# Kernel optimization log

Hardware: AMD Instinct MI355X
Metric: run time of the kernel (lower is better)

## Reference

```python
import jax, jax.numpy as jnp
import numpy as np

B = 2048

def _conv(x, w, b, stride):
    y = jax.lax.conv_general_dilated(x, w, (stride, stride), 'VALID',
                                     dimension_numbers=('NCHW', 'OIHW', 'NCHW'))
    return y + b[None, :, None, None]

def _local_conv(x, w, b):
    # w: (Ho, Wo, Co, Ci, kh, kw), b: (Ho, Wo, Co); stride 1, valid
    Ho, Wo, Co, Ci, kh, kw = w.shape
    # patches: (B, Ci, kh*kw, Ho, Wo) -- sliding windows, small fixed loop over kernel taps
    patches = jnp.stack([x[:, :, i:i + Ho, j:j + Wo]
                         for i in range(kh) for j in range(kw)], axis=2)
    wf = w.reshape(Ho, Wo, Co, Ci, kh * kw)
    y = jnp.einsum('bcphw,hwocp->bohw', patches, wf)
    return y + jnp.transpose(b, (2, 0, 1))[None]

def setup_inputs() -> dict:
    key = jax.random.key(0)
    ks = jax.random.split(key, 18)
    s = 0.05
    inp = {
        'x': jax.random.normal(ks[0], (B, 5, 60, 60), dtype=jnp.float32),
        'info': jax.random.normal(ks[1], (B, 8), dtype=jnp.float32),
        'w1': jax.random.normal(ks[2], (32, 5, 3, 3), dtype=jnp.float32) * s,
        'b1': jnp.zeros((32,), dtype=jnp.float32),
        'w2a': jax.random.normal(ks[3], (64, 32, 3, 3), dtype=jnp.float32) * s,
        'b2a': jnp.zeros((64,), dtype=jnp.float32),
        'w2b': jax.random.normal(ks[4], (64, 64, 3, 3), dtype=jnp.float32) * s,
        'b2b': jnp.zeros((64,), dtype=jnp.float32),
        'lw3': jax.random.normal(ks[5], (9, 9, 64, 64, 5, 5), dtype=jnp.float32) * s,
        'lb3': jnp.zeros((9, 9, 64), dtype=jnp.float32),
        'lw4': jax.random.normal(ks[6], (5, 5, 64, 64, 5, 5), dtype=jnp.float32) * s,
        'lb4': jnp.zeros((5, 5, 64), dtype=jnp.float32),
        'lw5': jax.random.normal(ks[7], (3, 3, 64, 64, 3, 3), dtype=jnp.float32) * s,
        'lb5': jnp.zeros((3, 3, 64), dtype=jnp.float32),
        'hw': jax.random.normal(ks[8], (2, 584), dtype=jnp.float32) * s,
        'hb': jnp.zeros((2,), dtype=jnp.float32),
    }
    return inp

def reference(x, info, w1, b1, w2a, b2a, w2b, b2b, lw3, lb3, lw4, lb4, lw5, lb5, hw, hb):
    h = jnp.tanh(_conv(x, w1, b1, 2))            # (B,32,29,29)
    h = jnp.tanh(_conv(h, w2a, b2a, 1))          # (B,64,27,27)
    h = jnp.tanh(_conv(h, w2b, b2b, 2))          # (B,64,13,13)
    h = jnp.tanh(_local_conv(h, lw3, lb3))       # (B,64,9,9)
    h = jnp.tanh(_local_conv(h, lw4, lb4))       # (B,64,5,5)
    h = jnp.tanh(_local_conv(h, lw5, lb5))       # (B,64,3,3)
    h = h.reshape(h.shape[0], -1)                # (B,576)
    h = jnp.concatenate([h, info], axis=1)       # (B,584)
    logits = h @ hw.T + hb                       # (B,2)
    return jax.nn.softmax(logits, axis=1)
```

## Files before the change

kernel.cpp:

```cpp
#include <hip/hip_runtime.h>
#include <stdint.h>

#define THREADS 256

typedef short bf16x8 __attribute__((ext_vector_type(8)));
typedef float f32x4 __attribute__((ext_vector_type(4)));
typedef unsigned uint2_ __attribute__((ext_vector_type(2)));

#define GPTR(x) ((const __attribute__((address_space(1))) void*)(x))
#define LPTR(x) ((__attribute__((address_space(3))) void*)(x))

__device__ __forceinline__ unsigned short f2bf(float v) {
  unsigned u = __builtin_bit_cast(unsigned, v);
  u = (u + 0x7fff + ((u >> 16) & 1)) >> 16;
  return (unsigned short)u;
}
__device__ __forceinline__ float bf2f(unsigned short h) {
  return __builtin_bit_cast(float, (unsigned)h << 16);
}
__device__ __forceinline__ float fast_tanh(float x) {
  return 1.f - 2.f / (__expf(2.f * x) + 1.f);
}

__device__ __forceinline__ int xcd_swizzle(int wg, int nwg) {
  const int q = nwg >> 3, rr = nwg & 7;
  const int xcd = wg & 7, l = wg >> 3;
  return (xcd < rr ? xcd * (q + 1) : rr * (q + 1) + (xcd - rr) * q) + l;
}

__global__ void pack_w1t(const float* __restrict__ w1, float* __restrict__ w1t) {
  int idx = blockIdx.x * THREADS + threadIdx.x;
  if (idx >= 45 * 32) return;
  int t = idx >> 5, co = idx & 31;
  w1t[t * 32 + co] = w1[co * 45 + t];
}

__global__ void __launch_bounds__(256) conv1_direct(
    const float* __restrict__ x, const float* __restrict__ w1t,
    const float* __restrict__ bias, unsigned short* __restrict__ out, int Bc,
    int bstart) {
  constexpr int CI = 5, CO = 32, IH = 60, IW = 60, OH = 29, OW = 29;
  constexpr int RPB = 2, NRB = 15;

  __shared__ float xs[CI * 5 * 60];

  const int tid = threadIdx.x;
  const int b = blockIdx.x / NRB;
  const int qb = blockIdx.x % NRB;
  const int oh0 = qb * RPB;
  const int rows = min(RPB, OH - oh0);
  const int ih0 = oh0 * 2;
  const int ihn = rows * 2 + 1;

  const float* xp = x + (size_t)(bstart + b) * (CI * IH * IW);

  const int nf4 = CI * ihn * 15;
  for (int i = tid; i < nf4; i += 256) {
    int col = i % 15;
    int row = i / 15;
    int ci = row / ihn, r = row % ihn;
    ((float4*)xs)[row * 15 + col] = ((const float4*)xp)[(ci * IH + ih0 + r) * 15 + col];
  }
  __syncthreads();

  const int lane = tid & 63;
  const int wu = __builtin_amdgcn_readfirstlane(tid >> 6);
  if (lane >= rows * OW) return;
  const int r = lane / OW, c = lane % OW;
  const int base = (r * 2) * 60 + c * 2;
  const int cstr = ihn * 60;

  float acc[8];
#pragma unroll
  for (int j = 0; j < 8; j++) acc[j] = bias[wu * 8 + j];

#pragma unroll
  for (int ci = 0; ci < CI; ci++)
#pragma unroll
    for (int kh = 0; kh < 3; kh++)
#pragma unroll
      for (int kw = 0; kw < 3; kw++) {
        const float v = xs[ci * cstr + base + kh * 60 + kw];
        const float* wt = w1t + ((ci * 3 + kh) * 3 + kw) * 32 + wu * 8;
#pragma unroll
        for (int j = 0; j < 8; j++) acc[j] = fmaf(v, wt[j], acc[j]);
      }

  const int p = (oh0 + r) * OW + c;
  bf16x8 o;
#pragma unroll
  for (int j = 0; j < 8; j++) o[j] = (short)f2bf(fast_tanh(acc[j]));
  *(bf16x8*)(out + ((size_t)p * Bc + b) * CO + wu * 8) = o;
}

template <int CI, int KS>
__global__ void __launch_bounds__(THREADS) pack_w(const float* __restrict__ w,
                                                  unsigned short* __restrict__ wp,
                                                  int npos) {
  constexpr int K = CI * KS * KS;
  constexpr int S = K / 32;
  int idx = blockIdx.x * THREADS + threadIdx.x;
  int total = npos * S * 2048;
  if (idx >= total) return;
  int e = idx & 7;
  int lane = (idx >> 3) & 63;
  int mt = (idx >> 9) & 3;
  int rest = idx >> 11;
  int s = rest % S, pos = rest / S;
  int co = mt * 16 + (lane & 15);
  int k = s * 32 + (lane >> 4) * 8 + e;
  int tap = k / CI, ci = k % CI;
  int kh = tap / KS, kw = tap % KS;
  float v = w[((((size_t)pos * 64 + co) * CI + ci) * KS + kh) * KS + kw];
  wp[idx] = f2bf(v);
}

template <int CI, int IH, int IW, int OH, int OW, int KS, int ST, bool LOCAL, int BT>
__global__ void __launch_bounds__(256) conv_mfma(
    const unsigned short* __restrict__ X, const unsigned short* __restrict__ Wp,
    const float* __restrict__ bias, unsigned short* __restrict__ Y, int Bc) {
  constexpr int S = CI * KS * KS / 32;
  constexpr int NPOS = OH * OW;
  constexpr int NJ = BT / 64;
  constexpr int NB = BT / 64;
  constexpr int NVM = 1 + NB;

  __shared__ unsigned short As[3][2048];
  __shared__ unsigned short Bs[3][BT * 32];

  const int tid = threadIdx.x;
  const int lane = tid & 63;
  const int wu = tid >> 6;
  const int n = lane & 15, g = lane >> 4;

  const int nbt = Bc / BT;
  int wg = xcd_swizzle(blockIdx.x, gridDim.x);
  int pos, btile;
  if (LOCAL) {
    btile = wg % nbt;
    pos = wg / nbt;
  } else {
    pos = wg % NPOS;
    btile = wg / NPOS;
  }
  const int oh = pos / OW, ow = pos % OW;
  const int b0 = btile * BT;

  const unsigned short* Wpp = Wp + (LOCAL ? (size_t)pos * (S * 2048) : 0);

  const int srow = tid >> 2;
  const int scol = (tid & 3) * 8;

  auto stage = [&](int s, int buf3) {
    __builtin_amdgcn_global_load_lds(GPTR(Wpp + s * 2048 + tid * 8),
                                     LPTR(&As[buf3][tid * 8]), 16, 0, 0);
    const int tap = (s * 32) / CI;
    const int ci0 = (s * 32) % CI;
    const int kh = tap / KS, kw = tap % KS;
    const int pin = (oh * ST + kh) * IW + (ow * ST + kw);
    const size_t base = (size_t)pin * Bc + b0;
#pragma unroll
    for (int i = 0; i < NB; i++)
      __builtin_amdgcn_global_load_lds(
          GPTR(X + (base + i * 64 + srow) * CI + ci0 + scol),
          LPTR(&Bs[buf3][i * 2048 + tid * 8]), 16, 0, 0);
  };

  f32x4 acc[4][NJ] = {};

  stage(0, 0);
  if (S > 1) stage(1, 1);
  int buf = 0;
  for (int s = 0; s < S; s++) {
    if (s + 1 < S)
      asm volatile("s_waitcnt vmcnt(%0)" ::"n"(NVM) : "memory");
    else
      asm volatile("s_waitcnt vmcnt(0)" ::: "memory");
    __builtin_amdgcn_s_barrier();
    __builtin_amdgcn_sched_barrier(0);
    if (s + 2 < S) stage(s + 2, buf == 0 ? 2 : buf - 1);

    bf16x8 bfr[NJ];
#pragma unroll
    for (int j = 0; j < NJ; j++) {
      const int local_b = wu * (NJ * 16) + j * 16 + n;
      bfr[j] = *(const bf16x8*)(&Bs[buf][local_b * 32 + g * 8]);
    }
    bf16x8 af[4];
#pragma unroll
    for (int mt = 0; mt < 4; mt++)
      af[mt] = *(const bf16x8*)(&As[buf][(mt * 64 + lane) * 8]);

#pragma unroll
    for (int mt = 0; mt < 4; mt++)
#pragma unroll
      for (int j = 0; j < NJ; j++)
        acc[mt][j] =
            __builtin_amdgcn_mfma_f32_16x16x32_bf16(af[mt], bfr[j], acc[mt][j], 0, 0, 0);
    buf = (buf == 2) ? 0 : buf + 1;
  }

#pragma unroll
  for (int mt = 0; mt < 4; mt++) {
#pragma unroll
    for (int j = 0; j < NJ; j++) {
      unsigned short o[4];
#pragma unroll
      for (int r = 0; r < 4; r++) {
        const int co = mt * 16 + g * 4 + r;
        o[r] = f2bf(fast_tanh(acc[mt][j][r] +
                              (LOCAL ? bias[pos * 64 + co] : bias[co])));
      }
      const int b = b0 + wu * (NJ * 16) + j * 16 + n;
      uint2_ pk;
      pk[0] = (unsigned)o[0] | ((unsigned)o[1] << 16);
      pk[1] = (unsigned)o[2] | ((unsigned)o[3] << 16);
      *(uint2_*)(Y + ((size_t)pos * Bc + b) * 64 + mt * 16 + g * 4) = pk;
    }
  }
}

__global__ void head_k(const unsigned short* __restrict__ h5,
                       const float* __restrict__ info, const float* __restrict__ hw,
                       const float* __restrict__ hb, float* __restrict__ out, int Bc,
                       int bstart) {
  int b = blockIdx.x * THREADS + threadIdx.x;
  if (b >= Bc) return;
  float l0 = hb[0], l1 = hb[1];
  for (int pos = 0; pos < 9; pos++) {
#pragma unroll
    for (int cb = 0; cb < 8; cb++) {
      bf16x8 v8 = *(const bf16x8*)(h5 + ((size_t)pos * Bc + b) * 64 + cb * 8);
#pragma unroll
      for (int j = 0; j < 8; j++) {
        float v = bf2f((unsigned short)v8[j]);
        int f = (cb * 8 + j) * 9 + pos;
        l0 = fmaf(v, hw[f], l0);
        l1 = fmaf(v, hw[584 + f], l1);
      }
    }
  }
#pragma unroll
  for (int k = 0; k < 8; k++) {
    float v = info[(size_t)(bstart + b) * 8 + k];
    l0 = fmaf(v, hw[576 + k], l0);
    l1 = fmaf(v, hw[584 + 576 + k], l1);
  }
  float m = fmaxf(l0, l1);
  float e0 = __expf(l0 - m), e1 = __expf(l1 - m);
  float s = e0 + e1;
  out[(size_t)(bstart + b) * 2 + 0] = e0 / s;
  out[(size_t)(bstart + b) * 2 + 1] = e1 / s;
}


extern "C" void kernel_launch(void* const* d_in, const int* in_sizes, int n_in,
                              void* d_out, int out_size, void* d_ws, size_t ws_size,
                              hipStream_t stream) {
  const float* x = (const float*)d_in[0];
  const float* info = (const float*)d_in[1];
  const float* w1 = (const float*)d_in[2];
  const float* b1 = (const float*)d_in[3];
  const float* w2a = (const float*)d_in[4];
  const float* b2a = (const float*)d_in[5];
  const float* w2b = (const float*)d_in[6];
  const float* b2b = (const float*)d_in[7];
  const float* lw3 = (const float*)d_in[8];
  const float* lb3 = (const float*)d_in[9];
  const float* lw4 = (const float*)d_in[10];
  const float* lb4 = (const float*)d_in[11];
  const float* lw5 = (const float*)d_in[12];
  const float* lb5 = (const float*)d_in[13];
  const float* hw = (const float*)d_in[14];
  const float* hb = (const float*)d_in[15];
  float* out = (float*)d_out;

  const int B = in_sizes[0] / 18000;

  const size_t SZ2A = 9ull * 2048, SZ2B = 18ull * 2048, SZ3 = 81ull * 50 * 2048,
               SZ4 = 25ull * 50 * 2048, SZ5 = 9ull * 18 * 2048;
  unsigned short* wp2a = (unsigned short*)d_ws;
  unsigned short* wp2b = wp2a + SZ2A;
  unsigned short* wp3 = wp2b + SZ2B;
  unsigned short* wp4 = wp3 + SZ3;
  unsigned short* wp5 = wp4 + SZ4;
  size_t wp_bytes = (SZ2A + SZ2B + SZ3 + SZ4 + SZ5) * 2;
  wp_bytes = (wp_bytes + 255) & ~(size_t)255;
  float* w1t = (float*)((char*)d_ws + wp_bytes);
  size_t w1t_bytes = ((45 * 32 * 4) + 255) & ~(size_t)255;

  const size_t PSA = 53824, PSB = 93312;
  const size_t per_sample = PSA + PSB;
  int Bc = B;
  while (Bc > 256 && wp_bytes + w1t_bytes + (size_t)Bc * per_sample + 4096 > ws_size)
    Bc >>= 1;

  char* base = (char*)d_ws + wp_bytes + w1t_bytes;
  unsigned short* bufA = (unsigned short*)base;
  unsigned short* bufB = (unsigned short*)(base + (size_t)Bc * PSA);

  hipLaunchKernelGGL(pack_w1t, dim3(6), dim3(THREADS), 0, stream, w1, w1t);
  hipLaunchKernelGGL((pack_w<32, 3>), dim3((SZ2A + 255) / 256), dim3(THREADS), 0, stream,
                     w2a, wp2a, 1);
  hipLaunchKernelGGL((pack_w<64, 3>), dim3((SZ2B + 255) / 256), dim3(THREADS), 0, stream,
                     w2b, wp2b, 1);
  hipLaunchKernelGGL((pack_w<64, 5>), dim3((SZ3 + 255) / 256), dim3(THREADS), 0, stream,
                     lw3, wp3, 81);
  hipLaunchKernelGGL((pack_w<64, 5>), dim3((SZ4 + 255) / 256), dim3(THREADS), 0, stream,
                     lw4, wp4, 25);
  hipLaunchKernelGGL((pack_w<64, 3>), dim3((SZ5 + 255) / 256), dim3(THREADS), 0, stream,
                     lw5, wp5, 9);

  const int nchunks = B / Bc;
  for (int c = 0; c < nchunks; c++) {
    const int bstart = c * Bc;

    hipLaunchKernelGGL(conv1_direct, dim3(Bc * 15), dim3(256), 0, stream, x, w1t, b1,
                       bufA, Bc, bstart);
    hipLaunchKernelGGL((conv_mfma<32, 29, 29, 27, 27, 3, 1, false, 256>),
                       dim3(729 * (Bc / 256)), dim3(256), 0, stream, bufA, wp2a, b2a,
                       bufB, Bc);
    hipLaunchKernelGGL((conv_mfma<64, 27, 27, 13, 13, 3, 2, false, 256>),
                       dim3(169 * (Bc / 256)), dim3(256), 0, stream, bufB, wp2b, b2b,
                       bufA, Bc);
    hipLaunchKernelGGL((conv_mfma<64, 13, 13, 9, 9, 5, 1, true, 256>),
                       dim3(81 * (Bc / 256)), dim3(256), 0, stream, bufA, wp3, lb3, bufB,
                       Bc);
    hipLaunchKernelGGL((conv_mfma<64, 9, 9, 5, 5, 5, 1, true, 128>),
                       dim3(25 * (Bc / 128)), dim3(256), 0, stream, bufB, wp4, lb4, bufA,
                       Bc);
    hipLaunchKernelGGL((conv_mfma<64, 5, 5, 3, 3, 3, 1, true, 128>),
                       dim3(9 * (Bc / 128)), dim3(256), 0, stream, bufA, wp5, lb5, bufB,
                       Bc);
    hipLaunchKernelGGL(head_k, dim3((Bc + THREADS - 1) / THREADS), dim3(THREADS), 0,
                       stream, bufB, info, hw, hb, out, Bc, bstart);
  }
}
```

Measured before the change: 576.0 us.

## Process several output positions per workgroup with a continuous cross-position pipeline

The shared-weight conv kernels now have each workgroup loop over a run of output positions (9 for conv2a, 3 for conv2b). The triple-buffered load pipeline carries across position boundaries, so prologue and epilogue stalls are paid once per run instead of once per position, and fewer workgroups are launched. The last local conv also moves to a 64-wide batch tile to launch more workgroups. In exchange the shared-weight conv grids become much smaller, which may reduce occupancy and load balance across CUs, and each run does serial epilogues.

```diff
diff --git a/kernel.cpp b/kernel.cpp
--- a/kernel.cpp
+++ b/kernel.cpp
@@ -115,7 +115,8 @@
   wp[idx] = f2bf(v);
 }
 
-template <int CI, int IH, int IW, int OH, int OW, int KS, int ST, bool LOCAL, int BT>
+template <int CI, int IH, int IW, int OH, int OW, int KS, int ST, bool LOCAL, int BT,
+          int NPOSB>
 __global__ void __launch_bounds__(256) conv_mfma(
     const unsigned short* __restrict__ X, const unsigned short* __restrict__ Wp,
     const float* __restrict__ bias, unsigned short* __restrict__ Y, int Bc) {
@@ -124,6 +125,7 @@
   constexpr int NJ = BT / 64;
   constexpr int NB = BT / 64;
   constexpr int NVM = 1 + NB;
+  constexpr int NRUNS = (NPOS + NPOSB - 1) / NPOSB;
 
   __shared__ unsigned short As[3][2048];
   __shared__ unsigned short Bs[3][BT * 32];
@@ -135,29 +137,34 @@
 
   const int nbt = Bc / BT;
   int wg = xcd_swizzle(blockIdx.x, gridDim.x);
-  int pos, btile;
+  int prun, btile;
   if (LOCAL) {
     btile = wg % nbt;
-    pos = wg / nbt;
+    prun = wg / nbt;
   } else {
-    pos = wg % NPOS;
-    btile = wg / NPOS;
-  }
-  const int oh = pos / OW, ow = pos % OW;
+    prun = wg % NRUNS;
+    btile = wg / NRUNS;
+  }
+  const int p0 = prun * NPOSB;
+  const int np = min(NPOSB, NPOS - p0);
   const int b0 = btile * BT;
-
-  const unsigned short* Wpp = Wp + (LOCAL ? (size_t)pos * (S * 2048) : 0);
+  const int T = np * S;
 
   const int srow = tid >> 2;
   const int scol = (tid & 3) * 8;
 
-  auto stage = [&](int s, int buf3) {
-    __builtin_amdgcn_global_load_lds(GPTR(Wpp + s * 2048 + tid * 8),
-                                     LPTR(&As[buf3][tid * 8]), 16, 0, 0);
-    const int tap = (s * 32) / CI;
-    const int ci0 = (s * 32) % CI;
+  auto stage = [&](int t, int buf3) {
+    const int pidx2 = t / S, s2 = t - pidx2 * S;
+    const int pos2 = p0 + pidx2;
+    const int oh2 = pos2 / OW, ow2 = pos2 % OW;
+    const unsigned short* Wpp =
+        Wp + (LOCAL ? (size_t)pos2 * (S * 2048) : 0) + (size_t)s2 * 2048;
+    __builtin_amdgcn_global_load_lds(GPTR(Wpp + tid * 8), LPTR(&As[buf3][tid * 8]), 16,
+                                     0, 0);
+    const int tap = (s2 * 32) / CI;
+    const int ci0 = (s2 * 32) % CI;
     const int kh = tap / KS, kw = tap % KS;
-    const int pin = (oh * ST + kh) * IW + (ow * ST + kw);
+    const int pin = (oh2 * ST + kh) * IW + (ow2 * ST + kw);
     const size_t base = (size_t)pin * Bc + b0;
 #pragma unroll
     for (int i = 0; i < NB; i++)
@@ -166,56 +173,60 @@
           LPTR(&Bs[buf3][i * 2048 + tid * 8]), 16, 0, 0);
   };
 
-  f32x4 acc[4][NJ] = {};
-
   stage(0, 0);
-  if (S > 1) stage(1, 1);
-  int buf = 0;
-  for (int s = 0; s < S; s++) {
-    if (s + 1 < S)
-      asm volatile("s_waitcnt vmcnt(%0)" ::"n"(NVM) : "memory");
-    else
-      asm volatile("s_waitcnt vmcnt(0)" ::: "memory");
-    __builtin_amdgcn_s_barrier();
-    __builtin_amdgcn_sched_barrier(0);
-    if (s + 2 < S) stage(s + 2, buf == 0 ? 2 : buf - 1);
-
-    bf16x8 bfr[NJ];
-#pragma unroll
-    for (int j = 0; j < NJ; j++) {
-      const int local_b = wu * (NJ * 16) + j * 16 + n;
-      bfr[j] = *(const bf16x8*)(&Bs[buf][local_b * 32 + g * 8]);
+  if (T > 1) stage(1, 1);
+
+  int t = 0;
+  for (int pidx = 0; pidx < np; pidx++) {
+    const int pos = p0 + pidx;
+    f32x4 acc[4][NJ] = {};
+
+    for (int s = 0; s < S; s++, t++) {
+      if (t + 1 < T)
+        asm volatile("s_waitcnt vmcnt(%0)" ::"n"(NVM) : "memory");
+      else
+        asm volatile("s_waitcnt vmcnt(0)" ::: "memory");
+      __builtin_amdgcn_s_barrier();
+      __builtin_amdgcn_sched_barrier(0);
+      if (t + 2 < T) stage(t + 2, (t + 2) % 3);
+
+      const int buf = t % 3;
+      bf16x8 bfr[NJ];
+#pragma unroll
+      for (int j = 0; j < NJ; j++) {
+        const int local_b = wu * (NJ * 16) + j * 16 + n;
+        bfr[j] = *(const bf16x8*)(&Bs[buf][local_b * 32 + g * 8]);
+      }
+      bf16x8 af[4];
+#pragma unroll
+      for (int mt = 0; mt < 4; mt++)
+        af[mt] = *(const bf16x8*)(&As[buf][(mt * 64 + lane) * 8]);
+
+#pragma unroll
+      for (int mt = 0; mt < 4; mt++)
+#pragma unroll
+        for (int j = 0; j < NJ; j++)
+          acc[mt][j] = __builtin_amdgcn_mfma_f32_16x16x32_bf16(af[mt], bfr[j],
+                                                               acc[mt][j], 0, 0, 0);
     }
-    bf16x8 af[4];
-#pragma unroll
-    for (int mt = 0; mt < 4; mt++)
-      af[mt] = *(const bf16x8*)(&As[buf][(mt * 64 + lane) * 8]);
-
-#pragma unroll
-    for (int mt = 0; mt < 4; mt++)
-#pragma unroll
-      for (int j = 0; j < NJ; j++)
-        acc[mt][j] =
-            __builtin_amdgcn_mfma_f32_16x16x32_bf16(af[mt], bfr[j], acc[mt][j], 0, 0, 0);
-    buf = (buf == 2) ? 0 : buf + 1;
-  }
-
-#pragma unroll
-  for (int mt = 0; mt < 4; mt++) {
-#pragma unroll
-    for (int j = 0; j < NJ; j++) {
-      unsigned short o[4];
-#pragma unroll
-      for (int r = 0; r < 4; r++) {
-        const int co = mt * 16 + g * 4 + r;
-        o[r] = f2bf(fast_tanh(acc[mt][j][r] +
-                              (LOCAL ? bias[pos * 64 + co] : bias[co])));
+
+#pragma unroll
+    for (int mt = 0; mt < 4; mt++) {
+#pragma unroll
+      for (int j = 0; j < NJ; j++) {
+        unsigned short o[4];
+#pragma unroll
+        for (int r = 0; r < 4; r++) {
+          const int co = mt * 16 + g * 4 + r;
+          o[r] = f2bf(
+              fast_tanh(acc[mt][j][r] + (LOCAL ? bias[pos * 64 + co] : bias[co])));
+        }
+        const int b = b0 + wu * (NJ * 16) + j * 16 + n;
+        uint2_ pk;
+        pk[0] = (unsigned)o[0] | ((unsigned)o[1] << 16);
+        pk[1] = (unsigned)o[2] | ((unsigned)o[3] << 16);
+        *(uint2_*)(Y + ((size_t)pos * Bc + b) * 64 + mt * 16 + g * 4) = pk;
       }
-      const int b = b0 + wu * (NJ * 16) + j * 16 + n;
-      uint2_ pk;
-      pk[0] = (unsigned)o[0] | ((unsigned)o[1] << 16);
-      pk[1] = (unsigned)o[2] | ((unsigned)o[3] << 16);
-      *(uint2_*)(Y + ((size_t)pos * Bc + b) * 64 + mt * 16 + g * 4) = pk;
     }
   }
 }
@@ -317,20 +328,20 @@
 
     hipLaunchKernelGGL(conv1_direct, dim3(Bc * 15), dim3(256), 0, stream, x, w1t, b1,
                        bufA, Bc, bstart);
-    hipLaunchKernelGGL((conv_mfma<32, 29, 29, 27, 27, 3, 1, false, 256>),
-                       dim3(729 * (Bc / 256)), dim3(256), 0, stream, bufA, wp2a, b2a,
+    hipLaunchKernelGGL((conv_mfma<32, 29, 29, 27, 27, 3, 1, false, 256, 9>),
+                       dim3(81 * (Bc / 256)), dim3(256), 0, stream, bufA, wp2a, b2a,
                        bufB, Bc);
-    hipLaunchKernelGGL((conv_mfma<64, 27, 27, 13, 13, 3, 2, false, 256>),
-                       dim3(169 * (Bc / 256)), dim3(256), 0, stream, bufB, wp2b, b2b,
+    hipLaunchKernelGGL((conv_mfma<64, 27, 27, 13, 13, 3, 2, false, 256, 3>),
+                       dim3(57 * (Bc / 256)), dim3(256), 0, stream, bufB, wp2b, b2b,
                        bufA, Bc);
-    hipLaunchKernelGGL((conv_mfma<64, 13, 13, 9, 9, 5, 1, true, 256>),
+    hipLaunchKernelGGL((conv_mfma<64, 13, 13, 9, 9, 5, 1, true, 256, 1>),
                        dim3(81 * (Bc / 256)), dim3(256), 0, stream, bufA, wp3, lb3, bufB,
                        Bc);
-    hipLaunchKernelGGL((conv_mfma<64, 9, 9, 5, 5, 5, 1, true, 128>),
+    hipLaunchKernelGGL((conv_mfma<64, 9, 9, 5, 5, 5, 1, true, 128, 1>),
                        dim3(25 * (Bc / 128)), dim3(256), 0, stream, bufB, wp4, lb4, bufA,
                        Bc);
-    hipLaunchKernelGGL((conv_mfma<64, 5, 5, 3, 3, 3, 1, true, 128>),
-                       dim3(9 * (Bc / 128)), dim3(256), 0, stream, bufA, wp5, lb5, bufB,
+    hipLaunchKernelGGL((conv_mfma<64, 5, 5, 3, 3, 3, 1, true, 64, 1>),
+                       dim3(9 * (Bc / 64)), dim3(256), 0, stream, bufA, wp5, lb5, bufB,
                        Bc);
     hipLaunchKernelGGL(head_k, dim3((Bc + THREADS - 1) / THREADS), dim3(THREADS), 0,
                        stream, bufB, info, hw, hb, out, Bc, bstart);
```

New measurement: 625.8 us. 8.6% more time.
